# Kernel tuning notes

Hardware: AMD Instinct MI355X
Metric: run time of the kernel (lower is better)

## Reference

```python
import jax, jax.numpy as jnp
import numpy as np

N_NODES = 50000
N_EDGES = 600000
D_IN, F1, F2, F3, D_OUT = 128, 128, 64, 64, 32
N_GRAPHS = 512


def setup_inputs() -> dict:
    key = jax.random.key(0)
    ks = jax.random.split(key, 16)
    x = jax.random.normal(ks[0], (N_NODES, D_IN), dtype=jnp.float32)
    edge_index = jax.random.randint(ks[1], (2, N_EDGES), 0, N_NODES, dtype=jnp.int64)
    batch = jnp.sort(jax.random.randint(ks[2], (N_NODES,), 0, N_GRAPHS, dtype=jnp.int64))

    def lin(k, fan_in, fan_out):
        bound = 1.0 / np.sqrt(fan_in)
        return jax.random.uniform(k, (fan_out, fan_in), jnp.float32, -bound, bound)

    return {
        "x": x, "edge_index": edge_index, "batch": batch,
        "w1_rel": lin(ks[3], D_IN, F1), "b1": jnp.zeros((F1,), jnp.float32), "w1_root": lin(ks[4], D_IN, F1),
        "w2_rel": lin(ks[5], F1, F2), "b2": jnp.zeros((F2,), jnp.float32), "w2_root": lin(ks[6], F1, F2),
        "w3_rel": lin(ks[7], F2, F3), "b3": jnp.zeros((F3,), jnp.float32), "w3_root": lin(ks[8], F2, F3),
        "fc1_w": lin(ks[9], F3, F3), "fc1_b": jnp.zeros((F3,), jnp.float32),
        "fc2_w": lin(ks[10], F3, D_OUT), "fc2_b": jnp.zeros((D_OUT,), jnp.float32),
    }


def graph_conv(x, src, dst, w_rel, b_rel, w_root):
    # GraphConv: out_i = W_rel @ (sum_{j->i} x_j) + b + W_root @ x_i
    aggr = jax.ops.segment_sum(x[src], dst, num_segments=x.shape[0])  # [N, d]
    return aggr @ w_rel.T + b_rel + x @ w_root.T


def reference(x, edge_index, batch,
              w1_rel, b1, w1_root, w2_rel, b2, w2_root, w3_rel, b3, w3_root,
              fc1_w, fc1_b, fc2_w, fc2_b):
    src, dst = edge_index[0], edge_index[1]
    h = jax.nn.relu(graph_conv(x, src, dst, w1_rel, b1, w1_root))
    h = jax.nn.relu(graph_conv(h, src, dst, w2_rel, b2, w2_root))
    h = graph_conv(h, src, dst, w3_rel, b3, w3_root)
    # global_add_pool over graphs in the batch
    g = jax.ops.segment_sum(h, batch, num_segments=N_GRAPHS)  # [G, F3]
    t = jax.nn.relu(g @ fc1_w.T + fc1_b)
    scores = t @ fc2_w.T + fc2_b
    return jax.nn.log_softmax(scores, axis=-1)
```

## Files before the change

### kernel.cpp

```cpp
#include <hip/hip_runtime.h>

#define N_NODES  50000
#define N_EDGES  600000
#define N_GRAPHS 512

#define SCAN_N   (N_NODES + 1)
#define SCAN_BPB 1024
#define SCAN_NB  ((SCAN_N + SCAN_BPB - 1) / SCAN_BPB)

typedef __attribute__((ext_vector_type(8))) short bf16x8;
typedef __attribute__((ext_vector_type(4))) float f32x4;

static __device__ __forceinline__ unsigned f2bf(float f) {
    unsigned u = __float_as_uint(f);
    return (u + 0x7FFFu + ((u >> 16) & 1u)) >> 16;
}
static __device__ __forceinline__ float bflo(unsigned v) { return __uint_as_float(v << 16); }
static __device__ __forceinline__ float bfhi(unsigned v) { return __uint_as_float(v & 0xFFFF0000u); }

static __device__ __forceinline__ void addv8(float* acc, uint4 v) {
    acc[0] += bflo(v.x); acc[1] += bfhi(v.x);
    acc[2] += bflo(v.y); acc[3] += bfhi(v.y);
    acc[4] += bflo(v.z); acc[5] += bfhi(v.z);
    acc[6] += bflo(v.w); acc[7] += bfhi(v.w);
}


__global__ void zero_int_kernel(int* __restrict__ p, int n) {
    int i = blockIdx.x * blockDim.x + threadIdx.x;
    if (i < n) p[i] = 0;
}
__global__ void zero_float_kernel(float* __restrict__ p, int n) {
    int i = blockIdx.x * blockDim.x + threadIdx.x;
    if (i < n) p[i] = 0.f;
}


__global__ void f2bf_kernel(const float* __restrict__ in, uint2* __restrict__ outp, int n4) {
    int i = blockIdx.x * blockDim.x + threadIdx.x;
    if (i >= n4) return;
    float4 v = ((const float4*)in)[i];
    uint2 o;
    o.x = f2bf(v.x) | (f2bf(v.y) << 16);
    o.y = f2bf(v.z) | (f2bf(v.w) << 16);
    outp[i] = o;
}

__global__ void wconv_kernel(const float* __restrict__ w1r, const float* __restrict__ w1o,
                             const float* __restrict__ w2r, const float* __restrict__ w2o,
                             const float* __restrict__ w3r, const float* __restrict__ w3o,
                             unsigned short* __restrict__ dst) {
    int i = blockIdx.x * blockDim.x + threadIdx.x;
    const float* src; int off;
    if      (i < 16384) { src = w1r; off = 0; }
    else if (i < 32768) { src = w1o; off = 16384; }
    else if (i < 40960) { src = w2r; off = 32768; }
    else if (i < 49152) { src = w2o; off = 40960; }
    else if (i < 53248) { src = w3r; off = 49152; }
    else if (i < 57344) { src = w3o; off = 53248; }
    else return;
    dst[i] = (unsigned short)f2bf(src[i - off]);
}


__global__ void hist_kernel(const int* __restrict__ edge, int* __restrict__ rowptr) {
    int e = blockIdx.x * blockDim.x + threadIdx.x;
    if (e < N_EDGES) atomicAdd(&rowptr[edge[N_EDGES + e] + 1], 1);
}

__global__ void scan_reduce_kernel(const int* __restrict__ data, int* __restrict__ bsum) {
    __shared__ int red[256];
    int b = blockIdx.x, t = threadIdx.x;
    int base = b * SCAN_BPB + t * 4;
    int s = 0;
#pragma unroll
    for (int j = 0; j < 4; ++j) {
        int idx = base + j;
        if (idx < SCAN_N) s += data[idx];
    }
    red[t] = s;
    __syncthreads();
    for (int off = 128; off > 0; off >>= 1) {
        if (t < off) red[t] += red[t + off];
        __syncthreads();
    }
    if (t == 0) bsum[b] = red[0];
}

__global__ void scan_sums_kernel(int* __restrict__ bsum) {
    __shared__ int sh[SCAN_NB];
    int t = threadIdx.x;
    if (t < SCAN_NB) sh[t] = bsum[t];
    __syncthreads();
    if (t == 0) {
        int run = 0;
        for (int i = 0; i < SCAN_NB; ++i) { int v = sh[i]; sh[i] = run; run += v; }
    }
    __syncthreads();
    if (t < SCAN_NB) bsum[t] = sh[t];
}

__global__ void scan_apply_kernel(int* __restrict__ data, const int* __restrict__ bexc,
                                  int* __restrict__ cursor) {
    __shared__ int th[256];
    int b = blockIdx.x, t = threadIdx.x;
    int base = b * SCAN_BPB + t * 4;
    int v[4];
    int s = 0;
#pragma unroll
    for (int j = 0; j < 4; ++j) {
        int idx = base + j;
        v[j] = (idx < SCAN_N) ? data[idx] : 0;
        s += v[j];
    }
    th[t] = s;
    __syncthreads();
    for (int off = 1; off < 256; off <<= 1) {
        int x = (t >= off) ? th[t - off] : 0;
        __syncthreads();
        th[t] += x;
        __syncthreads();
    }
    int run = bexc[b] + th[t] - s;
#pragma unroll
    for (int j = 0; j < 4; ++j) {
        int idx = base + j;
        run += v[j];
        if (idx < SCAN_N) {
            data[idx] = run;
            if (idx < N_NODES) cursor[idx] = run;
        }
    }
}

__global__ void scatter_kernel(const int* __restrict__ edge, int* __restrict__ cursor,
                               int* __restrict__ csr) {
    int e = blockIdx.x * blockDim.x + threadIdx.x;
    if (e < N_EDGES) {
        int d = edge[N_EDGES + e];
        int p = atomicAdd(&cursor[d], 1);
        csr[p] = edge[e];
    }
}

template <int LPN, int MODE>
__global__ void aggregate_u4(const unsigned short* __restrict__ Xb,
                             const int* __restrict__ rowptr,
                             const int* __restrict__ csr,
                             const unsigned short* __restrict__ ROOT,
                             void* __restrict__ OUT) {
    constexpr int NPB = 256 / LPN;
    int grp = threadIdx.x / LPN, lane = threadIdx.x % LPN;
    int i = blockIdx.x * NPB + grp;
    if (i >= N_NODES) return;
    const uint4* __restrict__ X4 = (const uint4*)Xb;
    int s = rowptr[i], e = rowptr[i + 1];
    float a[8] = {0.f}, b[8] = {0.f};
    int p = s;
    for (; p + 4 <= e; p += 4) {
        int j0 = csr[p + 0], j1 = csr[p + 1], j2 = csr[p + 2], j3 = csr[p + 3];
        uint4 v0 = X4[(size_t)j0 * LPN + lane];
        uint4 v1 = X4[(size_t)j1 * LPN + lane];
        uint4 v2 = X4[(size_t)j2 * LPN + lane];
        uint4 v3 = X4[(size_t)j3 * LPN + lane];
        addv8(a, v0); addv8(a, v1); addv8(b, v2); addv8(b, v3);
    }
    if (p + 2 <= e) {
        uint4 v0 = X4[(size_t)csr[p] * LPN + lane];
        uint4 v1 = X4[(size_t)csr[p + 1] * LPN + lane];
        addv8(a, v0); addv8(a, v1);
        p += 2;
    }
    if (p < e) {
        uint4 v = X4[(size_t)csr[p] * LPN + lane];
        addv8(b, v);
    }
    float f[8];
#pragma unroll
    for (int k = 0; k < 8; ++k) f[k] = a[k] + b[k];
    if constexpr (MODE != 0) {
        uint4 r = ((const uint4*)ROOT)[(size_t)i * LPN + lane];
        f[0] += bflo(r.x); f[1] += bfhi(r.x);
        f[2] += bflo(r.y); f[3] += bfhi(r.y);
        f[4] += bflo(r.z); f[5] += bfhi(r.z);
        f[6] += bflo(r.w); f[7] += bfhi(r.w);
    }
    if constexpr (MODE == 1) {
#pragma unroll
        for (int k = 0; k < 8; ++k) f[k] = fmaxf(f[k], 0.f);
    }
    if constexpr (MODE == 2) {
        float* row = (float*)OUT + (size_t)i * (LPN * 8) + lane * 8;
        *(float4*)row       = make_float4(f[0], f[1], f[2], f[3]);
        *(float4*)(row + 4) = make_float4(f[4], f[5], f[6], f[7]);
    } else {
        uint4 o;
        o.x = f2bf(f[0]) | (f2bf(f[1]) << 16);
        o.y = f2bf(f[2]) | (f2bf(f[3]) << 16);
        o.z = f2bf(f[4]) | (f2bf(f[5]) << 16);
        o.w = f2bf(f[6]) | (f2bf(f[7]) << 16);
        ((uint4*)OUT)[(size_t)i * LPN + lane] = o;
    }
}

template <int KS1, int KS2, int NT>
__launch_bounds__(256, 2)
__global__ void gemm_mfma(const unsigned short* __restrict__ A1,
                          const unsigned short* __restrict__ W1,
                          const unsigned short* __restrict__ A2,
                          const unsigned short* __restrict__ W2,
                          const float* __restrict__ bias,
                          unsigned short* __restrict__ OUT, int ldo) {
    constexpr int K1 = KS1 * 32, K2 = KS2 * 32;
    const int l  = threadIdx.x & 63;
    const int wv = threadIdx.x >> 6;
    const int lm = l & 15, lk = l >> 4;
    const int colbase = wv * (NT * 16);

    bf16x8 wf[NT][KS1 + KS2];
#pragma unroll
    for (int t = 0; t < NT; ++t) {
        int wrow = colbase + t * 16 + lm;
#pragma unroll
        for (int ks = 0; ks < KS1; ++ks)
            wf[t][ks] = *(const bf16x8*)(W1 + (size_t)wrow * K1 + ks * 32 + lk * 8);
#pragma unroll
        for (int ks = 0; ks < KS2; ++ks)
            wf[t][KS1 + ks] = *(const bf16x8*)(W2 + (size_t)wrow * K2 + ks * 32 + lk * 8);
    }

    int rt0 = blockIdx.x * 4;
    for (int r = 0; r < 4; ++r) {
        int rt = rt0 + r;
        if (rt >= N_NODES / 16) break;
        f32x4 acc[NT];
#pragma unroll
        for (int t = 0; t < NT; ++t) acc[t] = (f32x4){0.f, 0.f, 0.f, 0.f};

        const unsigned short* a1row = A1 + (size_t)(rt * 16 + lm) * K1 + lk * 8;
#pragma unroll
        for (int ks = 0; ks < KS1; ++ks) {
            bf16x8 a = *(const bf16x8*)(a1row + ks * 32);
#pragma unroll
            for (int t = 0; t < NT; ++t)
                acc[t] = __builtin_amdgcn_mfma_f32_16x16x32_bf16(a, wf[t][ks], acc[t], 0, 0, 0);
        }
        const unsigned short* a2row = A2 + (size_t)(rt * 16 + lm) * K2 + lk * 8;
#pragma unroll
        for (int ks = 0; ks < KS2; ++ks) {
            bf16x8 a = *(const bf16x8*)(a2row + ks * 32);
#pragma unroll
            for (int t = 0; t < NT; ++t)
                acc[t] = __builtin_amdgcn_mfma_f32_16x16x32_bf16(a, wf[t][KS1 + ks], acc[t], 0, 0, 0);
        }
#pragma unroll
        for (int t = 0; t < NT; ++t) {
            int n = colbase + t * 16 + lm;
            float bv = bias[n];
#pragma unroll
            for (int j = 0; j < 4; ++j) {
                int m = rt * 16 + lk * 4 + j;
                float v = fmaxf(acc[t][j] + bv, 0.f);
                OUT[(size_t)m * ldo + n] = (unsigned short)f2bf(v);
            }
        }
    }
}

template <int KS>
__launch_bounds__(256, 2)
__global__ void gemm_dual(const unsigned short* __restrict__ A,
                          const unsigned short* __restrict__ W,
                          const float* __restrict__ bias,
                          unsigned short* __restrict__ OUTY,
                          unsigned short* __restrict__ OUTR) {
    constexpr int K = KS * 32, NT = 2;
    const int l  = threadIdx.x & 63;
    const int wv = threadIdx.x >> 6;
    const int lm = l & 15, lk = l >> 4;
    const int colbase = wv * (NT * 16);

    bf16x8 wf[NT][KS];
#pragma unroll
    for (int t = 0; t < NT; ++t) {
        int wrow = colbase + t * 16 + lm;
#pragma unroll
        for (int ks = 0; ks < KS; ++ks)
            wf[t][ks] = *(const bf16x8*)(W + (size_t)wrow * K + ks * 32 + lk * 8);
    }

    int rt0 = blockIdx.x * 4;
    for (int r = 0; r < 4; ++r) {
        int rt = rt0 + r;
        if (rt >= N_NODES / 16) break;
        f32x4 acc[NT];
#pragma unroll
        for (int t = 0; t < NT; ++t) acc[t] = (f32x4){0.f, 0.f, 0.f, 0.f};

        const unsigned short* arow = A + (size_t)(rt * 16 + lm) * K + lk * 8;
#pragma unroll
        for (int ks = 0; ks < KS; ++ks) {
            bf16x8 a = *(const bf16x8*)(arow + ks * 32);
#pragma unroll
            for (int t = 0; t < NT; ++t)
                acc[t] = __builtin_amdgcn_mfma_f32_16x16x32_bf16(a, wf[t][ks], acc[t], 0, 0, 0);
        }
#pragma unroll
        for (int t = 0; t < NT; ++t) {
            int n = colbase + t * 16 + lm;
#pragma unroll
            for (int j = 0; j < 4; ++j) {
                int m = rt * 16 + lk * 4 + j;
                float v = acc[t][j];
                if (n < 64) {
                    OUTY[(size_t)m * 64 + n] = (unsigned short)f2bf(v);
                } else {
                    v += bias[n - 64];
                    OUTR[(size_t)m * 64 + (n - 64)] = (unsigned short)f2bf(v);
                }
            }
        }
    }
}


__global__ void pool_kernel(const float* __restrict__ H, const int* __restrict__ batch,
                            float* __restrict__ G, int n) {
    const int CHUNK = 128;
    int f = threadIdx.x;
    int start = blockIdx.x * CHUNK;
    if (start >= n) return;
    int end = start + CHUNK; if (end > n) end = n;
    int cur = batch[start];
    float acc = 0.f;
    for (int i = start; i < end; ++i) {
        int b = batch[i];
        if (b != cur) { atomicAdd(&G[(size_t)cur * 64 + f], acc); acc = 0.f; cur = b; }
        acc += H[(size_t)i * 64 + f];
    }
    atomicAdd(&G[(size_t)cur * 64 + f], acc);
}


__global__ void mlp_head(const float* __restrict__ G, const float* __restrict__ fc1w,
                         const float* __restrict__ fc1b, const float* __restrict__ fc2w,
                         const float* __restrict__ fc2b, float* __restrict__ out) {
    int g = blockIdx.x;
    int t = threadIdx.x;
    __shared__ float gr[64], tt[64], sc[32], red[2];
    gr[t] = G[(size_t)g * 64 + t];
    __syncthreads();
    float acc = fc1b[t];
#pragma unroll
    for (int k = 0; k < 64; ++k) acc += gr[k] * fc1w[t * 64 + k];
    tt[t] = fmaxf(acc, 0.f);
    __syncthreads();
    if (t < 32) {
        float s = fc2b[t];
#pragma unroll
        for (int k = 0; k < 64; ++k) s += tt[k] * fc2w[t * 64 + k];
        sc[t] = s;
    }
    __syncthreads();
    if (t == 0) {
        float mx = sc[0];
        for (int c = 1; c < 32; ++c) mx = fmaxf(mx, sc[c]);
        float sum = 0.f;
        for (int c = 0; c < 32; ++c) sum += expf(sc[c] - mx);
        red[0] = mx; red[1] = logf(sum);
    }
    __syncthreads();
    if (t < 32) out[(size_t)g * 32 + t] = sc[t] - red[0] - red[1];
}


extern "C" void kernel_launch(void* const* d_in, const int* in_sizes, int n_in,
                              void* d_out, int out_size, void* d_ws, size_t ws_size,
                              hipStream_t stream) {
    const float* x       = (const float*)d_in[0];
    const int*   edge    = (const int*)d_in[1];
    const int*   batch   = (const int*)d_in[2];
    const float* w1_rel  = (const float*)d_in[3];
    const float* b1      = (const float*)d_in[4];
    const float* w1_root = (const float*)d_in[5];
    const float* w2_rel  = (const float*)d_in[6];
    const float* b2      = (const float*)d_in[7];
    const float* w2_root = (const float*)d_in[8];
    const float* w3_rel  = (const float*)d_in[9];
    const float* b3      = (const float*)d_in[10];
    const float* w3_root = (const float*)d_in[11];
    const float* fc1w    = (const float*)d_in[12];
    const float* fc1b    = (const float*)d_in[13];
    const float* fc2w    = (const float*)d_in[14];
    const float* fc2b    = (const float*)d_in[15];
    float* out = (float*)d_out;

    char* p = (char*)d_ws;
    size_t used = 0;
    auto alloc = [&](size_t bytes) {
        char* r = p + used;
        used += (bytes + 255) & ~(size_t)255;
        return r;
    };
    int*            rowptr = (int*)alloc((N_NODES + 1) * sizeof(int));
    int*            cursor = (int*)alloc(N_NODES * sizeof(int));
    int*            csr    = (int*)alloc(N_EDGES * sizeof(int));
    int*            bsum   = (int*)alloc(SCAN_NB * sizeof(int));
    unsigned short* wbf    = (unsigned short*)alloc(57344 * sizeof(unsigned short));
    unsigned short* bufX   = (unsigned short*)alloc((size_t)N_NODES * 128 * 2);
    unsigned short* bufA   = (unsigned short*)alloc((size_t)N_NODES * 128 * 2);
    unsigned short* bufH   = (unsigned short*)alloc((size_t)N_NODES * 128 * 2);
    float*          G      = (float*)alloc((size_t)N_GRAPHS * 64 * sizeof(float));

    if (used > ws_size) return;

    unsigned short* w1r_bf = wbf;
    unsigned short* w1o_bf = wbf + 16384;
    unsigned short* w2cat  = wbf + 32768;
    unsigned short* w3cat  = wbf + 49152;

    unsigned short* XB    = bufX;
    unsigned short* AGG1b = bufA;
    unsigned short* H1b   = bufH;
    unsigned short* Y2B   = bufX;
    unsigned short* ROOT2 = bufX + (size_t)N_NODES * 64;
    unsigned short* H2b   = bufA;
    unsigned short* Y3B   = bufX;
    unsigned short* ROOT3 = bufX + (size_t)N_NODES * 64;
    float*          H3    = (float*)bufH;

    zero_int_kernel<<<(N_NODES + 256) / 256, 256, 0, stream>>>(rowptr, N_NODES + 1);
    hist_kernel<<<(N_EDGES + 255) / 256, 256, 0, stream>>>(edge, rowptr);
    scan_reduce_kernel<<<SCAN_NB, 256, 0, stream>>>(rowptr, bsum);
    scan_sums_kernel<<<1, 64, 0, stream>>>(bsum);
    scan_apply_kernel<<<SCAN_NB, 256, 0, stream>>>(rowptr, bsum, cursor);
    scatter_kernel<<<(N_EDGES + 255) / 256, 256, 0, stream>>>(edge, cursor, csr);

    f2bf_kernel<<<(N_NODES * 32 + 255) / 256, 256, 0, stream>>>(x, (uint2*)XB, N_NODES * 32);
    wconv_kernel<<<224, 256, 0, stream>>>(w1_rel, w1_root, w2_rel, w2_root, w3_rel, w3_root, wbf);

    int gblk = (N_NODES / 16 + 3) / 4;

    aggregate_u4<16, 0><<<(N_NODES + 15) / 16, 256, 0, stream>>>(XB, rowptr, csr, nullptr, AGG1b);
    gemm_mfma<4, 4, 2><<<gblk, 256, 0, stream>>>(AGG1b, w1r_bf, XB, w1o_bf, b1, H1b, 128);

    gemm_dual<4><<<gblk, 256, 0, stream>>>(H1b, w2cat, b2, Y2B, ROOT2);
    aggregate_u4<8, 1><<<(N_NODES + 31) / 32, 256, 0, stream>>>(Y2B, rowptr, csr, ROOT2, H2b);

    gemm_dual<2><<<gblk, 256, 0, stream>>>(H2b, w3cat, b3, Y3B, ROOT3);
    aggregate_u4<8, 2><<<(N_NODES + 31) / 32, 256, 0, stream>>>(Y3B, rowptr, csr, ROOT3, H3);

    zero_float_kernel<<<(N_GRAPHS * 64 + 255) / 256, 256, 0, stream>>>(G, N_GRAPHS * 64);
    pool_kernel<<<(N_NODES + 127) / 128, 64, 0, stream>>>(H3, batch, G, N_NODES);
    mlp_head<<<N_GRAPHS, 64, 0, stream>>>(G, fc1w, fc1b, fc2w, fc2b, out);
}
```

Baseline: 321.7 us.

## Fuse init kernels, fold scan sums into apply, deepen gather unroll, per-graph pooling

Merges the x bf16 conversion, rowptr zeroing and weight conversion into one init kernel. The scan-sums kernel is dropped, and each scan_apply block now sums the preceding block totals itself. The aggregation loop is unrolled to 8 neighbours to keep more gathers in flight. Pooling becomes one block per graph that binary-searches the sorted batch array and writes directly, removing the zeroing kernel and the atomics. The aim is fewer launches and more memory-level parallelism, at the cost of serial per-block prefix loops and possible load imbalance across graphs.

```diff
diff --git a/kernel.cpp b/kernel.cpp
--- a/kernel.cpp
+++ b/kernel.cpp
@@ -7,6 +7,10 @@
 #define SCAN_N   (N_NODES + 1)
 #define SCAN_BPB 1024
 #define SCAN_NB  ((SCAN_N + SCAN_BPB - 1) / SCAN_BPB)
+
+#define F2BF_BLOCKS 6250
+#define ZR_BLOCKS   196
+#define WC_BLOCKS   224
 
 typedef __attribute__((ext_vector_type(8))) short bf16x8;
 typedef __attribute__((ext_vector_type(4))) float f32x4;
@@ -26,40 +30,35 @@
 }
 
 
-__global__ void zero_int_kernel(int* __restrict__ p, int n) {
-    int i = blockIdx.x * blockDim.x + threadIdx.x;
-    if (i < n) p[i] = 0;
-}
-__global__ void zero_float_kernel(float* __restrict__ p, int n) {
-    int i = blockIdx.x * blockDim.x + threadIdx.x;
-    if (i < n) p[i] = 0.f;
-}
-
-
-__global__ void f2bf_kernel(const float* __restrict__ in, uint2* __restrict__ outp, int n4) {
-    int i = blockIdx.x * blockDim.x + threadIdx.x;
-    if (i >= n4) return;
-    float4 v = ((const float4*)in)[i];
-    uint2 o;
-    o.x = f2bf(v.x) | (f2bf(v.y) << 16);
-    o.y = f2bf(v.z) | (f2bf(v.w) << 16);
-    outp[i] = o;
-}
-
-__global__ void wconv_kernel(const float* __restrict__ w1r, const float* __restrict__ w1o,
-                             const float* __restrict__ w2r, const float* __restrict__ w2o,
-                             const float* __restrict__ w3r, const float* __restrict__ w3o,
-                             unsigned short* __restrict__ dst) {
-    int i = blockIdx.x * blockDim.x + threadIdx.x;
-    const float* src; int off;
-    if      (i < 16384) { src = w1r; off = 0; }
-    else if (i < 32768) { src = w1o; off = 16384; }
-    else if (i < 40960) { src = w2r; off = 32768; }
-    else if (i < 49152) { src = w2o; off = 40960; }
-    else if (i < 53248) { src = w3r; off = 49152; }
-    else if (i < 57344) { src = w3o; off = 53248; }
-    else return;
-    dst[i] = (unsigned short)f2bf(src[i - off]);
+__global__ void init_kernel(const float* __restrict__ x, uint2* __restrict__ xb,
+                            int* __restrict__ rowptr,
+                            const float* __restrict__ w1r, const float* __restrict__ w1o,
+                            const float* __restrict__ w2r, const float* __restrict__ w2o,
+                            const float* __restrict__ w3r, const float* __restrict__ w3o,
+                            unsigned short* __restrict__ wdst) {
+    int b = blockIdx.x, t = threadIdx.x;
+    if (b < F2BF_BLOCKS) {
+        int i = b * 256 + t;
+        float4 v = ((const float4*)x)[i];
+        uint2 o;
+        o.x = f2bf(v.x) | (f2bf(v.y) << 16);
+        o.y = f2bf(v.z) | (f2bf(v.w) << 16);
+        xb[i] = o;
+    } else if (b < F2BF_BLOCKS + ZR_BLOCKS) {
+        int i = (b - F2BF_BLOCKS) * 256 + t;
+        if (i < SCAN_N) rowptr[i] = 0;
+    } else {
+        int i = (b - F2BF_BLOCKS - ZR_BLOCKS) * 256 + t;
+        const float* src; int off;
+        if      (i < 16384) { src = w1r; off = 0; }
+        else if (i < 32768) { src = w1o; off = 16384; }
+        else if (i < 40960) { src = w2r; off = 32768; }
+        else if (i < 49152) { src = w2o; off = 40960; }
+        else if (i < 53248) { src = w3r; off = 49152; }
+        else if (i < 57344) { src = w3o; off = 53248; }
+        else return;
+        wdst[i] = (unsigned short)f2bf(src[i - off]);
+    }
 }
 
 
@@ -87,23 +86,16 @@
     if (t == 0) bsum[b] = red[0];
 }
 
-__global__ void scan_sums_kernel(int* __restrict__ bsum) {
-    __shared__ int sh[SCAN_NB];
-    int t = threadIdx.x;
-    if (t < SCAN_NB) sh[t] = bsum[t];
-    __syncthreads();
+__global__ void scan_apply_kernel(int* __restrict__ data, const int* __restrict__ bsum,
+                                  int* __restrict__ cursor) {
+    __shared__ int th[256];
+    __shared__ int boff;
+    int b = blockIdx.x, t = threadIdx.x;
     if (t == 0) {
         int run = 0;
-        for (int i = 0; i < SCAN_NB; ++i) { int v = sh[i]; sh[i] = run; run += v; }
-    }
-    __syncthreads();
-    if (t < SCAN_NB) bsum[t] = sh[t];
-}
-
-__global__ void scan_apply_kernel(int* __restrict__ data, const int* __restrict__ bexc,
-                                  int* __restrict__ cursor) {
-    __shared__ int th[256];
-    int b = blockIdx.x, t = threadIdx.x;
+        for (int i = 0; i < b; ++i) run += bsum[i];
+        boff = run;
+    }
     int base = b * SCAN_BPB + t * 4;
     int v[4];
     int s = 0;
@@ -121,7 +113,7 @@
         th[t] += x;
         __syncthreads();
     }
-    int run = bexc[b] + th[t] - s;
+    int run = boff + th[t] - s;
 #pragma unroll
     for (int j = 0; j < 4; ++j) {
         int idx = base + j;
@@ -157,23 +149,35 @@
     int s = rowptr[i], e = rowptr[i + 1];
     float a[8] = {0.f}, b[8] = {0.f};
     int p = s;
-    for (; p + 4 <= e; p += 4) {
-        int j0 = csr[p + 0], j1 = csr[p + 1], j2 = csr[p + 2], j3 = csr[p + 3];
-        uint4 v0 = X4[(size_t)j0 * LPN + lane];
-        uint4 v1 = X4[(size_t)j1 * LPN + lane];
-        uint4 v2 = X4[(size_t)j2 * LPN + lane];
-        uint4 v3 = X4[(size_t)j3 * LPN + lane];
-        addv8(a, v0); addv8(a, v1); addv8(b, v2); addv8(b, v3);
+    for (; p + 8 <= e; p += 8) {
+        uint4 v0 = X4[(size_t)csr[p + 0] * LPN + lane];
+        uint4 v1 = X4[(size_t)csr[p + 1] * LPN + lane];
+        uint4 v2 = X4[(size_t)csr[p + 2] * LPN + lane];
+        uint4 v3 = X4[(size_t)csr[p + 3] * LPN + lane];
+        uint4 v4 = X4[(size_t)csr[p + 4] * LPN + lane];
+        uint4 v5 = X4[(size_t)csr[p + 5] * LPN + lane];
+        uint4 v6 = X4[(size_t)csr[p + 6] * LPN + lane];
+        uint4 v7 = X4[(size_t)csr[p + 7] * LPN + lane];
+        addv8(a, v0); addv8(b, v1); addv8(a, v2); addv8(b, v3);
+        addv8(a, v4); addv8(b, v5); addv8(a, v6); addv8(b, v7);
+    }
+    if (p + 4 <= e) {
+        uint4 v0 = X4[(size_t)csr[p + 0] * LPN + lane];
+        uint4 v1 = X4[(size_t)csr[p + 1] * LPN + lane];
+        uint4 v2 = X4[(size_t)csr[p + 2] * LPN + lane];
+        uint4 v3 = X4[(size_t)csr[p + 3] * LPN + lane];
+        addv8(a, v0); addv8(b, v1); addv8(a, v2); addv8(b, v3);
+        p += 4;
     }
     if (p + 2 <= e) {
         uint4 v0 = X4[(size_t)csr[p] * LPN + lane];
         uint4 v1 = X4[(size_t)csr[p + 1] * LPN + lane];
-        addv8(a, v0); addv8(a, v1);
+        addv8(a, v0); addv8(b, v1);
         p += 2;
     }
     if (p < e) {
         uint4 v = X4[(size_t)csr[p] * LPN + lane];
-        addv8(b, v);
+        addv8(a, v);
     }
     float f[8];
 #pragma unroll
@@ -202,6 +206,7 @@
         ((uint4*)OUT)[(size_t)i * LPN + lane] = o;
     }
 }
+
 
 template <int KS1, int KS2, int NT>
 __launch_bounds__(256, 2)
@@ -324,21 +329,19 @@
 }
 
 
-__global__ void pool_kernel(const float* __restrict__ H, const int* __restrict__ batch,
-                            float* __restrict__ G, int n) {
-    const int CHUNK = 128;
-    int f = threadIdx.x;
-    int start = blockIdx.x * CHUNK;
-    if (start >= n) return;
-    int end = start + CHUNK; if (end > n) end = n;
-    int cur = batch[start];
+__global__ void pool_graph(const float* __restrict__ H, const int* __restrict__ batch,
+                           float* __restrict__ G) {
+    int g = blockIdx.x;
+    int t = threadIdx.x;
+    int lo = 0, hi = N_NODES;
+    while (lo < hi) { int mid = (lo + hi) >> 1; if (batch[mid] < g) lo = mid + 1; else hi = mid; }
+    int start = lo;
+    hi = N_NODES;
+    while (lo < hi) { int mid = (lo + hi) >> 1; if (batch[mid] < g + 1) lo = mid + 1; else hi = mid; }
+    int end = lo;
     float acc = 0.f;
-    for (int i = start; i < end; ++i) {
-        int b = batch[i];
-        if (b != cur) { atomicAdd(&G[(size_t)cur * 64 + f], acc); acc = 0.f; cur = b; }
-        acc += H[(size_t)i * 64 + f];
-    }
-    atomicAdd(&G[(size_t)cur * 64 + f], acc);
+    for (int i = start; i < end; ++i) acc += H[(size_t)i * 64 + t];
+    G[(size_t)g * 64 + t] = acc;
 }
 
 
@@ -429,16 +432,14 @@
     unsigned short* ROOT3 = bufX + (size_t)N_NODES * 64;
     float*          H3    = (float*)bufH;
 
-    zero_int_kernel<<<(N_NODES + 256) / 256, 256, 0, stream>>>(rowptr, N_NODES + 1);
+    init_kernel<<<F2BF_BLOCKS + ZR_BLOCKS + WC_BLOCKS, 256, 0, stream>>>(
+        x, (uint2*)XB, rowptr, w1_rel, w1_root, w2_rel, w2_root, w3_rel, w3_root, wbf);
+
     hist_kernel<<<(N_EDGES + 255) / 256, 256, 0, stream>>>(edge, rowptr);
     scan_reduce_kernel<<<SCAN_NB, 256, 0, stream>>>(rowptr, bsum);
-    scan_sums_kernel<<<1, 64, 0, stream>>>(bsum);
     scan_apply_kernel<<<SCAN_NB, 256, 0, stream>>>(rowptr, bsum, cursor);
     scatter_kernel<<<(N_EDGES + 255) / 256, 256, 0, stream>>>(edge, cursor, csr);
 
-    f2bf_kernel<<<(N_NODES * 32 + 255) / 256, 256, 0, stream>>>(x, (uint2*)XB, N_NODES * 32);
-    wconv_kernel<<<224, 256, 0, stream>>>(w1_rel, w1_root, w2_rel, w2_root, w3_rel, w3_root, wbf);
-
     int gblk = (N_NODES / 16 + 3) / 4;
 
     aggregate_u4<16, 0><<<(N_NODES + 15) / 16, 256, 0, stream>>>(XB, rowptr, csr, nullptr, AGG1b);
@@ -450,7 +451,6 @@
     gemm_dual<2><<<gblk, 256, 0, stream>>>(H2b, w3cat, b3, Y3B, ROOT3);
     aggregate_u4<8, 2><<<(N_NODES + 31) / 32, 256, 0, stream>>>(Y3B, rowptr, csr, ROOT3, H3);
 
-    zero_float_kernel<<<(N_GRAPHS * 64 + 255) / 256, 256, 0, stream>>>(G, N_GRAPHS * 64);
-    pool_kernel<<<(N_NODES + 127) / 128, 64, 0, stream>>>(H3, batch, G, N_NODES);
+    pool_graph<<<N_GRAPHS, 64, 0, stream>>>(H3, batch, G);
     mlp_head<<<N_GRAPHS, 64, 0, stream>>>(G, fc1w, fc1b, fc2w, fc2b, out);
 }
```

New measurement: 324.1 us. About the same (+0.8%).
